# Performance work log

Hardware: AMD Instinct MI355X
Metric: run time of the kernel (lower is better)

Reference implementation:

```python
import jax, jax.numpy as jnp
import numpy as np

N_NODES = 12000
N_EDGES = 384000
F_IN = 128       # num_features
D = 64           # latent_dim (hidden_dim), num_gc_layers = 1
H_DEC = 64       # ceil(F_IN / 2)
BN_EPS = 1e-4


def _gcn_conv(x, W, b, src, dst, n):
    # PyG GCNConv: h = x @ W; add self-loops; sym-normalized scatter-add; + bias
    h = x @ W
    loop = jnp.arange(n)
    s = jnp.concatenate([src, loop])
    d = jnp.concatenate([dst, loop])
    deg = jax.ops.segment_sum(jnp.ones(s.shape[0], dtype=x.dtype), d, num_segments=n)
    dis = jax.lax.rsqrt(deg)  # deg >= 1 thanks to self-loops
    norm = dis[s] * dis[d]    # [E+N]
    out = jax.ops.segment_sum(h[s] * norm[:, None], d, num_segments=n)
    return out + b


def _bn_train(x, gamma, beta):
    # BatchNorm1d, training-mode batch statistics, biased variance, eps=1e-4
    mu = jnp.mean(x, axis=0)
    xc = x - mu
    var = jnp.mean(xc * xc, axis=0)
    return xc * jax.lax.rsqrt(var + BN_EPS) * gamma + beta


def _enc_layer(x, W, b, g, be, src, dst, n):
    # GCNConv -> Sigmoid -> (dropout no-op) -> BatchNorm
    return _bn_train(jax.nn.sigmoid(_gcn_conv(x, W, b, src, dst, n)), g, be)


def setup_inputs() -> dict:
    key = jax.random.key(0)
    ks = jax.random.split(key, 16)
    inp = {
        'x': jax.random.normal(ks[0], (N_NODES, F_IN), dtype=jnp.float32),
        'src': jax.random.randint(ks[1], (N_EDGES,), 0, N_NODES),
        'dst': jax.random.randint(ks[2], (N_EDGES,), 0, N_NODES),
        'batch': jnp.zeros((N_NODES,), dtype=jnp.int32),
        'noise': jax.random.normal(ks[3], (N_NODES, D), dtype=jnp.float32),
        # base_gcn encoder (GCNConv F_IN -> D, BN)
        'W0': jax.random.normal(ks[4], (F_IN, D), dtype=jnp.float32) * 0.08,
        'b0': jnp.zeros((D,), dtype=jnp.float32),
        'g0': jnp.ones((D,), dtype=jnp.float32),
        'be0': jnp.zeros((D,), dtype=jnp.float32),
        # gcn_mean encoder (GCNConv D -> D, BN)
        'Wm': jax.random.normal(ks[5], (D, D), dtype=jnp.float32) * 0.12,
        'bm': jnp.zeros((D,), dtype=jnp.float32),
        'gm': jnp.ones((D,), dtype=jnp.float32),
        'bem': jnp.zeros((D,), dtype=jnp.float32),
        # gcn_logstddev encoder (GCNConv D -> D, BN)
        'Ws': jax.random.normal(ks[6], (D, D), dtype=jnp.float32) * 0.12,
        'bs': jnp.zeros((D,), dtype=jnp.float32),
        'gs': jnp.ones((D,), dtype=jnp.float32),
        'bes': jnp.zeros((D,), dtype=jnp.float32),
        # decoder MLP: Linear(D, H_DEC) -> LeakyReLU -> Linear(H_DEC, F_IN)
        'Dw1': jax.random.normal(ks[7], (D, H_DEC), dtype=jnp.float32) * 0.12,
        'Db1': jnp.zeros((H_DEC,), dtype=jnp.float32),
        'Dw2': jax.random.normal(ks[8], (H_DEC, F_IN), dtype=jnp.float32) * 0.12,
        'Db2': jnp.zeros((F_IN,), dtype=jnp.float32),
    }
    return inp


def reference(x, src, dst, batch, noise,
              W0, b0, g0, be0,
              Wm, bm, gm, bem,
              Ws, bs, gs, bes,
              Dw1, Db1, Dw2, Db2):
    n = x.shape[0]
    hidden = _enc_layer(x, W0, b0, g0, be0, src, dst, n)          # [N, D]
    mean = _enc_layer(hidden, Wm, bm, gm, bem, src, dst, n)       # [N, D]
    logstd = _enc_layer(hidden, Ws, bs, gs, bes, src, dst, n)     # [N, D]
    z = noise * jnp.exp(logstd) + mean                            # reparam trick
    # decoder MLP (LeakyReLU default slope 0.01)
    h = jax.nn.leaky_relu(z @ Dw1 + Db1, negative_slope=0.01)
    reconstructed_x = h @ Dw2 + Db2                               # [N, F_IN]
    A_pred = jax.nn.sigmoid(z @ z.T)                              # [N, N]
    return (reconstructed_x, A_pred)
```

## Files before the change

kernel.cpp:

```cpp
#include <hip/hip_runtime.h>
#include <hip/hip_bf16.h>

#define N_NODES 12000
#define N_EDGES 384000
#define F_INN   128
#define DLAT    64
#define BN_EPS  1e-4f

typedef __attribute__((ext_vector_type(8))) short bf16x8;
typedef __attribute__((ext_vector_type(4))) float f32x4;

__device__ __forceinline__ float sigmoidf(float x) { return 1.0f / (1.0f + __expf(-x)); }

__device__ __forceinline__ unsigned short f2bf_rne(float x) {
    unsigned u = __float_as_uint(x);
    unsigned r = (u + 0x7fffu + ((u >> 16) & 1u)) >> 16;
    return (unsigned short)r;
}
__device__ __forceinline__ float bf2f(unsigned short h) {
    return __uint_as_float((unsigned)h << 16);
}

__global__ void k_init(int* cnt, int* cur, int n) {
    int i = blockIdx.x * blockDim.x + threadIdx.x;
    if (i < n) { cnt[i] = 0; cur[i] = 0; }
}

__global__ void k_count(const int* dst, int* cnt, int e) {
    int i = blockIdx.x * blockDim.x + threadIdx.x;
    if (i < e) atomicAdd(&cnt[dst[i]], 1);
}

__global__ void k_scan(const int* __restrict__ cnt, int* __restrict__ offs,
                       float* __restrict__ dis, int n) {
    __shared__ int wsum[16];
    int tid = threadIdx.x;
    int base = tid * 12;
    int v[12];
    int s = 0;
#pragma unroll
    for (int q = 0; q < 12; q++) {
        int i = base + q;
        v[q] = (i < n) ? cnt[i] : 0;
        s += v[q];
        if (i < n) dis[i] = rsqrtf((float)(v[q] + 1));
    }
    int lane = tid & 63, w = tid >> 6;
    int ps = s;
#pragma unroll
    for (int o = 1; o < 64; o <<= 1) {
        int t2 = __shfl_up(ps, o, 64);
        if (lane >= o) ps += t2;
    }
    if (lane == 63) wsum[w] = ps;
    __syncthreads();
    if (tid == 0) {
        int acc = 0;
        for (int i = 0; i < 16; i++) { int t2 = wsum[i]; wsum[i] = acc; acc += t2; }
    }
    __syncthreads();
    int acc = wsum[w] + ps - s;
#pragma unroll
    for (int q = 0; q < 12; q++) {
        int i = base + q;
        if (i < n) offs[i] = acc;
        acc += v[q];
        if (i == n - 1) offs[n] = acc;
    }
}

__global__ void k_scatter(const int* src, const int* dst, const int* offs, int* cur,
                          int* ssrc, int e) {
    int i = blockIdx.x * blockDim.x + threadIdx.x;
    if (i < e) {
        int d = dst[i];
        int p = atomicAdd(&cur[d], 1);
        ssrc[offs[d] + p] = src[i];
    }
}

__global__ void k_mm(const float* __restrict__ X, int n, int K,
                     const float* __restrict__ Wa, int Ma,
                     const float* __restrict__ Wb, int Mb,
                     float* __restrict__ out) {
    __shared__ float Wl[8192];
    int M = Ma + Mb;
    for (int idx = threadIdx.x; idx < K * M; idx += blockDim.x) {
        int k = idx / M, m = idx % M;
        Wl[idx] = (m < Ma) ? Wa[k * Ma + m] : Wb[k * Mb + (m - Ma)];
    }
    __syncthreads();
    int rpb = blockDim.x / M;
    int r = blockIdx.x * rpb + threadIdx.x / M;
    int m = threadIdx.x % M;
    if (r >= n) return;
    const float* xr = X + (size_t)r * K;
    float acc = 0.f;
    for (int k = 0; k < K; k++) acc += xr[k] * Wl[k * M + m];
    out[(size_t)r * M + m] = acc;
}

__global__ void k_agg(const float* __restrict__ h, const float* __restrict__ dis,
                      const int* __restrict__ offs, const int* __restrict__ ssrc,
                      const float* __restrict__ ba, const float* __restrict__ bb, int Ma,
                      float* __restrict__ out, int dim, int n) {
    int t = blockIdx.x * blockDim.x + threadIdx.x;
    int node = t / dim;
    if (node >= n) return;
    int f = t - node * dim;
    float di = dis[node];
    float acc = h[(size_t)node * dim + f] * di;
    int e0 = offs[node], e1 = offs[node + 1];
    int j = e0;
    for (; j + 3 < e1; j += 4) {
        int s0 = ssrc[j], s1 = ssrc[j + 1], s2 = ssrc[j + 2], s3 = ssrc[j + 3];
        acc += h[(size_t)s0 * dim + f] * dis[s0];
        acc += h[(size_t)s1 * dim + f] * dis[s1];
        acc += h[(size_t)s2 * dim + f] * dis[s2];
        acc += h[(size_t)s3 * dim + f] * dis[s3];
    }
    for (; j < e1; j++) {
        int s = ssrc[j];
        acc += h[(size_t)s * dim + f] * dis[s];
    }
    float bias = (f < Ma) ? ba[f] : bb[f - Ma];
    out[(size_t)node * dim + f] = sigmoidf(acc * di + bias);
}

#define STATS_BLOCKS 64
__global__ void k_stats1(const float* __restrict__ act, int dim, int n,
                         float* __restrict__ part) {
    int rpb = 256 / dim;
    int c = threadIdx.x % dim;
    int rloc = threadIdx.x / dim;
    float s = 0.f, s2 = 0.f;
    for (int r = blockIdx.x * rpb + rloc; r < n; r += STATS_BLOCKS * rpb) {
        float v = act[(size_t)r * dim + c];
        s += v; s2 += v * v;
    }
    __shared__ float sh[512];
    sh[threadIdx.x] = s; sh[256 + threadIdx.x] = s2;
    __syncthreads();
    if (rloc == 0) {
        for (int q = 1; q < rpb; q++) {
            s += sh[q * dim + c];
            s2 += sh[256 + q * dim + c];
        }
        part[(size_t)(blockIdx.x * dim + c) * 2] = s;
        part[(size_t)(blockIdx.x * dim + c) * 2 + 1] = s2;
    }
}

__global__ void k_stats2(const float* __restrict__ part, int dim, int n,
                         float* __restrict__ mu, float* __restrict__ var) {
    int c = threadIdx.x;
    if (c >= dim) return;
    float s = 0.f, s2 = 0.f;
    for (int q = 0; q < STATS_BLOCKS; q++) {
        s += part[(size_t)(q * dim + c) * 2];
        s2 += part[(size_t)(q * dim + c) * 2 + 1];
    }
    float m = s / n;
    mu[c] = m;
    var[c] = s2 / n - m * m;
}

__global__ void k_bnapply(const float* __restrict__ in, float* __restrict__ out,
                          const float* __restrict__ mu, const float* __restrict__ var,
                          const float* __restrict__ g, const float* __restrict__ be,
                          int dim, size_t total) {
    size_t i = (size_t)blockIdx.x * blockDim.x + threadIdx.x;
    if (i >= total) return;
    int f = (int)(i % dim);
    out[i] = (in[i] - mu[f]) * rsqrtf(var[f] + BN_EPS) * g[f] + be[f];
}

__global__ void k_z(const float* __restrict__ act2, const float* __restrict__ noise,
                    const float* __restrict__ mu, const float* __restrict__ var,
                    const float* __restrict__ gm, const float* __restrict__ bem,
                    const float* __restrict__ gs, const float* __restrict__ bes,
                    float* __restrict__ z, unsigned short* __restrict__ zh,
                    unsigned short* __restrict__ zl, int n) {
    int i = blockIdx.x * blockDim.x + threadIdx.x;
    if (i >= 12032 * 64) return;
    int row = i >> 6, j = i & 63;
    if (row >= n) { zh[i] = 0; zl[i] = 0; return; }
    const float* ar = act2 + (size_t)row * 128;
    float m  = (ar[j]      - mu[j])      * rsqrtf(var[j]      + BN_EPS) * gm[j] + bem[j];
    float ls = (ar[j + 64] - mu[j + 64]) * rsqrtf(var[j + 64] + BN_EPS) * gs[j] + bes[j];
    float zv = noise[i] * __expf(ls) + m;
    z[i] = zv;
    unsigned short h = f2bf_rne(zv);
    zh[i] = h;
    zl[i] = f2bf_rne(zv - bf2f(h));
}

__global__ void k_dec(const float* __restrict__ z,
                      const float* __restrict__ W1, const float* __restrict__ B1,
                      const float* __restrict__ W2, const float* __restrict__ B2,
                      float* __restrict__ out, int n) {
    __shared__ float w1[64 * 64];
    __shared__ float w2[64 * 128];
    __shared__ float zl[16 * 64];
    __shared__ float hl[16 * 64];
    int t = threadIdx.x;
    int row0 = blockIdx.x * 16;
    {
        const float4* W14 = (const float4*)W1;
        const float4* W24 = (const float4*)W2;
        for (int i = t; i < 1024; i += 256) ((float4*)w1)[i] = W14[i];
        for (int i = t; i < 2048; i += 256) ((float4*)w2)[i] = W24[i];
        ((float4*)zl)[t] = ((const float4*)(z + (size_t)row0 * 64))[t];
    }
    __syncthreads();
    {
        int hc = t & 63, rg = t >> 6;
        float a0 = B1[hc], a1 = a0, a2 = a0, a3 = a0;
        int rb = rg * 4;
        for (int k = 0; k < 64; k++) {
            float wv = w1[k * 64 + hc];
            a0 += zl[(rb + 0) * 64 + k] * wv;
            a1 += zl[(rb + 1) * 64 + k] * wv;
            a2 += zl[(rb + 2) * 64 + k] * wv;
            a3 += zl[(rb + 3) * 64 + k] * wv;
        }
        hl[(rb + 0) * 64 + hc] = a0 > 0.f ? a0 : 0.01f * a0;
        hl[(rb + 1) * 64 + hc] = a1 > 0.f ? a1 : 0.01f * a1;
        hl[(rb + 2) * 64 + hc] = a2 > 0.f ? a2 : 0.01f * a2;
        hl[(rb + 3) * 64 + hc] = a3 > 0.f ? a3 : 0.01f * a3;
    }
    __syncthreads();
    {
        int oc = t & 127, rg = t >> 7;
        float o[8];
#pragma unroll
        for (int i = 0; i < 8; i++) o[i] = B2[oc];
        int rb = rg * 8;
        for (int k = 0; k < 64; k++) {
            float wv = w2[k * 128 + oc];
#pragma unroll
            for (int i = 0; i < 8; i++) o[i] += hl[(rb + i) * 64 + k] * wv;
        }
#pragma unroll
        for (int i = 0; i < 8; i++)
            out[(size_t)(row0 + rb + i) * 128 + oc] = o[i];
    }
}

#define TN2 94
__global__ __launch_bounds__(256, 2) void k_apred(const unsigned short* __restrict__ zh,
                                                  const unsigned short* __restrict__ zl,
                                                  float* __restrict__ out, int n) {
    __shared__ __align__(16) unsigned short si_h[128 * 64];
    __shared__ __align__(16) unsigned short si_l[128 * 64];
    __shared__ __align__(16) unsigned short sj_h[128 * 64];
    __shared__ __align__(16) unsigned short sj_l[128 * 64];

    int bj = blockIdx.x, bi = blockIdx.y;
    int i0 = bi * 128, j0 = bj * 128;
    int t = threadIdx.x;

    auto stage = [&](const unsigned short* __restrict__ g, unsigned short* s, int row0) {
#pragma unroll
        for (int q = 0; q < 4; q++) {
            int u = q * 256 + t;
            int row = u >> 3, c16 = u & 7;
            int c16s = c16 ^ (row & 7);
            *(float4*)((char*)s + row * 128 + c16s * 16) =
                *(const float4*)(g + (size_t)(row0 + row) * 64 + c16 * 8);
        }
    };
    stage(zh, si_h, i0);
    stage(zl, si_l, i0);
    stage(zh, sj_h, j0);
    stage(zl, sj_l, j0);
    __syncthreads();

    int wave = t >> 6, lane = t & 63;
    int wr = wave >> 1, wc = wave & 1;
    int lrow = lane & 15;
    int kg   = lane >> 4;

    auto frag = [&](const unsigned short* s, int tr, int kc) -> bf16x8 {
        int c16s = (kc * 4 + kg) ^ (tr & 7);
        return *(const bf16x8*)((const char*)s + tr * 128 + c16s * 16);
    };

    f32x4 acc[4][4] = {};

#pragma unroll
    for (int kc = 0; kc < 2; kc++) {
        bf16x8 ah[4], al[4], bh[4], bl[4];
#pragma unroll
        for (int f = 0; f < 4; f++) {
            int tra = wr * 64 + f * 16 + lrow;
            ah[f] = frag(si_h, tra, kc);
            al[f] = frag(si_l, tra, kc);
            int trb = wc * 64 + f * 16 + lrow;
            bh[f] = frag(sj_h, trb, kc);
            bl[f] = frag(sj_l, trb, kc);
        }
#pragma unroll
        for (int fi = 0; fi < 4; fi++)
#pragma unroll
            for (int fj = 0; fj < 4; fj++) {
                acc[fi][fj] = __builtin_amdgcn_mfma_f32_16x16x32_bf16(
                    ah[fi], bh[fj], acc[fi][fj], 0, 0, 0);
                acc[fi][fj] = __builtin_amdgcn_mfma_f32_16x16x32_bf16(
                    ah[fi], bl[fj], acc[fi][fj], 0, 0, 0);
                acc[fi][fj] = __builtin_amdgcn_mfma_f32_16x16x32_bf16(
                    al[fi], bh[fj], acc[fi][fj], 0, 0, 0);
            }
    }

#pragma unroll
    for (int fi = 0; fi < 4; fi++)
#pragma unroll
        for (int fj = 0; fj < 4; fj++)
#pragma unroll
            for (int q = 0; q < 4; q++)
                acc[fi][fj][q] = sigmoidf(acc[fi][fj][q]);

    int colb = j0 + wc * 64;
#pragma unroll
    for (int fi = 0; fi < 4; fi++) {
#pragma unroll
        for (int q = 0; q < 4; q++) {
            int r = i0 + wr * 64 + fi * 16 + kg * 4 + q;
            if (r < n) {
                float* orow = out + (size_t)r * n + colb;
#pragma unroll
                for (int fj = 0; fj < 4; fj++) {
                    int c = fj * 16 + lrow;
                    if (colb + c < n) orow[c] = acc[fi][fj][q];
                }
            }
        }
    }
}

extern "C" void kernel_launch(void* const* d_in, const int* in_sizes, int n_in,
                              void* d_out, int out_size, void* d_ws, size_t ws_size,
                              hipStream_t stream) {
    const float* x     = (const float*)d_in[0];
    const int*   src   = (const int*)d_in[1];
    const int*   dst   = (const int*)d_in[2];
    const float* noise = (const float*)d_in[4];
    const float* W0  = (const float*)d_in[5];
    const float* b0  = (const float*)d_in[6];
    const float* g0  = (const float*)d_in[7];
    const float* be0 = (const float*)d_in[8];
    const float* Wm  = (const float*)d_in[9];
    const float* bm  = (const float*)d_in[10];
    const float* gm  = (const float*)d_in[11];
    const float* bem = (const float*)d_in[12];
    const float* Ws  = (const float*)d_in[13];
    const float* bs  = (const float*)d_in[14];
    const float* gs  = (const float*)d_in[15];
    const float* bes = (const float*)d_in[16];
    const float* Dw1 = (const float*)d_in[17];
    const float* Db1 = (const float*)d_in[18];
    const float* Dw2 = (const float*)d_in[19];
    const float* Db2 = (const float*)d_in[20];
    float* out = (float*)d_out;

    const int n = N_NODES, e = N_EDGES;

    int*   cnt  = (int*)d_ws;
    int*   offs = (int*)d_ws + 12032;
    int*   cur  = (int*)d_ws + 24064;
    int*   ssrc = (int*)d_ws + 36096;
    float* dis  = (float*)d_ws + 420096;
    float* mu   = (float*)d_ws + 432128;
    float* var  = (float*)d_ws + 432384;
    float* part = (float*)d_ws + 432640;
    float* bufA = (float*)d_ws + 449024;
    float* bufB = bufA + (size_t)N_NODES * 128;
    float* zbuf = bufB;
    unsigned short* zhbuf = (unsigned short*)((float*)d_ws + 3521024);
    unsigned short* zlbuf = (unsigned short*)((float*)d_ws + 3906048);

    k_init<<<(n + 255) / 256, 256, 0, stream>>>(cnt, cur, n);
    k_count<<<(e + 255) / 256, 256, 0, stream>>>(dst, cnt, e);
    k_scan<<<1, 1024, 0, stream>>>(cnt, offs, dis, n);
    k_scatter<<<(e + 255) / 256, 256, 0, stream>>>(src, dst, offs, cur, ssrc, e);

    k_mm<<<n / 4, 256, 0, stream>>>(x, n, F_INN, W0, DLAT, nullptr, 0, bufA);
    k_agg<<<(n * DLAT) / 256, 256, 0, stream>>>(bufA, dis, offs, ssrc, b0, nullptr, DLAT,
                                                bufB, DLAT, n);
    k_stats1<<<STATS_BLOCKS, 256, 0, stream>>>(bufB, DLAT, n, part);
    k_stats2<<<1, 64, 0, stream>>>(part, DLAT, n, mu, var);
    k_bnapply<<<(n * DLAT) / 256, 256, 0, stream>>>(bufB, bufA, mu, var, g0, be0, DLAT,
                                                    (size_t)n * DLAT);

    k_mm<<<n / 2, 256, 0, stream>>>(bufA, n, DLAT, Wm, DLAT, Ws, DLAT, bufB);
    k_agg<<<(n * 128) / 256, 256, 0, stream>>>(bufB, dis, offs, ssrc, bm, bs, DLAT,
                                               bufA, 128, n);
    k_stats1<<<STATS_BLOCKS, 256, 0, stream>>>(bufA, 128, n, part);
    k_stats2<<<1, 128, 0, stream>>>(part, 128, n, mu, var);

    k_z<<<(12032 * 64) / 256, 256, 0, stream>>>(bufA, noise, mu, var, gm, bem, gs, bes,
                                                zbuf, zhbuf, zlbuf, n);

    k_dec<<<n / 16, 256, 0, stream>>>(zbuf, Dw1, Db1, Dw2, Db2, out, n);

    {
        dim3 grid(TN2, TN2);
        k_apred<<<grid, 256, 0, stream>>>(zhbuf, zlbuf, out + (size_t)n * F_INN, n);
    }
}
```

Measured before the change: 952.6 us.

## Fuse BatchNorm apply into matmul and z/decoder kernels, use atomic stats

Drops the separate stats-finalize, BN-apply and z kernels. BN statistics are accumulated with atomics into a zeroed buffer, the first BN is folded into the following matmul's input load, and the second BN plus the reparameterization are computed inside the decoder kernel, which also writes the bf16 hi/lo z arrays. The large A_pred output now uses nontemporal stores. This cuts kernel launches and intermediate round trips to memory, but float atomics make the reduction order nondeterministic.

```diff
diff --git a/kernel.cpp b/kernel.cpp
--- a/kernel.cpp
+++ b/kernel.cpp
@@ -21,9 +21,16 @@
     return __uint_as_float((unsigned)h << 16);
 }
 
-__global__ void k_init(int* cnt, int* cur, int n) {
+__global__ void k_init(int* cnt, int* cur, float* sA, float* sB,
+                       unsigned short* zh, unsigned short* zl, int n) {
     int i = blockIdx.x * blockDim.x + threadIdx.x;
     if (i < n) { cnt[i] = 0; cur[i] = 0; }
+    if (i < 128) sA[i] = 0.f;
+    if (i < 256) sB[i] = 0.f;
+    if (i < 2048) {
+        zh[12000 * 64 + i] = 0;
+        zl[12000 * 64 + i] = 0;
+    }
 }
 
 __global__ void k_count(const int* dst, int* cnt, int e) {
@@ -98,6 +105,39 @@
     float acc = 0.f;
     for (int k = 0; k < K; k++) acc += xr[k] * Wl[k * M + m];
     out[(size_t)r * M + m] = acc;
+}
+
+__global__ void k_mm2bn(const float* __restrict__ X,
+                        const float* __restrict__ sums,
+                        const float* __restrict__ g0, const float* __restrict__ be0,
+                        const float* __restrict__ Wa, const float* __restrict__ Wb,
+                        float* __restrict__ out, int n) {
+    __shared__ float Wl[64 * 128];
+    __shared__ float bna[64], bnc[64];
+    __shared__ float xs[2 * 64];
+    int t = threadIdx.x;
+    for (int idx = t; idx < 64 * 128; idx += 256) {
+        int k = idx >> 7, m = idx & 127;
+        Wl[idx] = (m < 64) ? Wa[k * 64 + m] : Wb[k * 64 + (m - 64)];
+    }
+    if (t < 64) {
+        float mu = sums[t] / n;
+        float var = sums[64 + t] / n - mu * mu;
+        float a = rsqrtf(var + BN_EPS) * g0[t];
+        bna[t] = a;
+        bnc[t] = be0[t] - mu * a;
+    }
+    __syncthreads();
+    if (t < 128) {
+        int rr = t >> 6, k = t & 63;
+        xs[rr * 64 + k] = X[(size_t)(blockIdx.x * 2 + rr) * 64 + k] * bna[k] + bnc[k];
+    }
+    __syncthreads();
+    int r_loc = t >> 7, m = t & 127;
+    int r = blockIdx.x * 2 + r_loc;
+    float acc = 0.f;
+    for (int k = 0; k < 64; k++) acc += xs[r_loc * 64 + k] * Wl[k * 128 + m];
+    out[(size_t)r * 128 + m] = acc;
 }
 
 __global__ void k_agg(const float* __restrict__ h, const float* __restrict__ dis,
@@ -129,7 +169,7 @@
 
 #define STATS_BLOCKS 64
 __global__ void k_stats1(const float* __restrict__ act, int dim, int n,
-                         float* __restrict__ part) {
+                         float* __restrict__ sums) {
     int rpb = 256 / dim;
     int c = threadIdx.x % dim;
     int rloc = threadIdx.x / dim;
@@ -146,63 +186,24 @@
             s += sh[q * dim + c];
             s2 += sh[256 + q * dim + c];
         }
-        part[(size_t)(blockIdx.x * dim + c) * 2] = s;
-        part[(size_t)(blockIdx.x * dim + c) * 2 + 1] = s2;
-    }
-}
-
-__global__ void k_stats2(const float* __restrict__ part, int dim, int n,
-                         float* __restrict__ mu, float* __restrict__ var) {
-    int c = threadIdx.x;
-    if (c >= dim) return;
-    float s = 0.f, s2 = 0.f;
-    for (int q = 0; q < STATS_BLOCKS; q++) {
-        s += part[(size_t)(q * dim + c) * 2];
-        s2 += part[(size_t)(q * dim + c) * 2 + 1];
-    }
-    float m = s / n;
-    mu[c] = m;
-    var[c] = s2 / n - m * m;
-}
-
-__global__ void k_bnapply(const float* __restrict__ in, float* __restrict__ out,
-                          const float* __restrict__ mu, const float* __restrict__ var,
-                          const float* __restrict__ g, const float* __restrict__ be,
-                          int dim, size_t total) {
-    size_t i = (size_t)blockIdx.x * blockDim.x + threadIdx.x;
-    if (i >= total) return;
-    int f = (int)(i % dim);
-    out[i] = (in[i] - mu[f]) * rsqrtf(var[f] + BN_EPS) * g[f] + be[f];
-}
-
-__global__ void k_z(const float* __restrict__ act2, const float* __restrict__ noise,
-                    const float* __restrict__ mu, const float* __restrict__ var,
-                    const float* __restrict__ gm, const float* __restrict__ bem,
-                    const float* __restrict__ gs, const float* __restrict__ bes,
-                    float* __restrict__ z, unsigned short* __restrict__ zh,
-                    unsigned short* __restrict__ zl, int n) {
-    int i = blockIdx.x * blockDim.x + threadIdx.x;
-    if (i >= 12032 * 64) return;
-    int row = i >> 6, j = i & 63;
-    if (row >= n) { zh[i] = 0; zl[i] = 0; return; }
-    const float* ar = act2 + (size_t)row * 128;
-    float m  = (ar[j]      - mu[j])      * rsqrtf(var[j]      + BN_EPS) * gm[j] + bem[j];
-    float ls = (ar[j + 64] - mu[j + 64]) * rsqrtf(var[j + 64] + BN_EPS) * gs[j] + bes[j];
-    float zv = noise[i] * __expf(ls) + m;
-    z[i] = zv;
-    unsigned short h = f2bf_rne(zv);
-    zh[i] = h;
-    zl[i] = f2bf_rne(zv - bf2f(h));
-}
-
-__global__ void k_dec(const float* __restrict__ z,
-                      const float* __restrict__ W1, const float* __restrict__ B1,
-                      const float* __restrict__ W2, const float* __restrict__ B2,
-                      float* __restrict__ out, int n) {
+        atomicAdd(&sums[c], s);
+        atomicAdd(&sums[dim + c], s2);
+    }
+}
+
+__global__ void k_zdec(const float* __restrict__ act2, const float* __restrict__ noise,
+                       const float* __restrict__ sums,
+                       const float* __restrict__ gm, const float* __restrict__ bem,
+                       const float* __restrict__ gs, const float* __restrict__ bes,
+                       const float* __restrict__ W1, const float* __restrict__ B1,
+                       const float* __restrict__ W2, const float* __restrict__ B2,
+                       unsigned short* __restrict__ zh, unsigned short* __restrict__ zl,
+                       float* __restrict__ out, int n) {
     __shared__ float w1[64 * 64];
     __shared__ float w2[64 * 128];
-    __shared__ float zl[16 * 64];
+    __shared__ float zs[16 * 64];
     __shared__ float hl[16 * 64];
+    __shared__ float bnS[128], bnC[128];
     int t = threadIdx.x;
     int row0 = blockIdx.x * 16;
     {
@@ -210,7 +211,35 @@
         const float4* W24 = (const float4*)W2;
         for (int i = t; i < 1024; i += 256) ((float4*)w1)[i] = W14[i];
         for (int i = t; i < 2048; i += 256) ((float4*)w2)[i] = W24[i];
-        ((float4*)zl)[t] = ((const float4*)(z + (size_t)row0 * 64))[t];
+    }
+    if (t < 128) {
+        float mu = sums[t] / n;
+        float var = sums[128 + t] / n - mu * mu;
+        float rs = rsqrtf(var + BN_EPS);
+        float g  = (t < 64) ? gm[t] : gs[t - 64];
+        float be = (t < 64) ? bem[t] : bes[t - 64];
+        float a = rs * g;
+        bnS[t] = a;
+        bnC[t] = be - mu * a;
+    }
+    __syncthreads();
+    {
+        int base = t * 4;
+        int row = base >> 6, j0 = base & 63;
+        const float* ar = act2 + (size_t)(row0 + row) * 128;
+        const float* nr = noise + (size_t)(row0 + row) * 64;
+#pragma unroll
+        for (int q = 0; q < 4; q++) {
+            int j = j0 + q;
+            float m  = ar[j]      * bnS[j]      + bnC[j];
+            float ls = ar[64 + j] * bnS[64 + j] + bnC[64 + j];
+            float zv = nr[j] * __expf(ls) + m;
+            zs[row * 64 + j] = zv;
+            unsigned short h = f2bf_rne(zv);
+            size_t gi = (size_t)(row0 + row) * 64 + j;
+            zh[gi] = h;
+            zl[gi] = f2bf_rne(zv - bf2f(h));
+        }
     }
     __syncthreads();
     {
@@ -219,10 +248,10 @@
         int rb = rg * 4;
         for (int k = 0; k < 64; k++) {
             float wv = w1[k * 64 + hc];
-            a0 += zl[(rb + 0) * 64 + k] * wv;
-            a1 += zl[(rb + 1) * 64 + k] * wv;
-            a2 += zl[(rb + 2) * 64 + k] * wv;
-            a3 += zl[(rb + 3) * 64 + k] * wv;
+            a0 += zs[(rb + 0) * 64 + k] * wv;
+            a1 += zs[(rb + 1) * 64 + k] * wv;
+            a2 += zs[(rb + 2) * 64 + k] * wv;
+            a3 += zs[(rb + 3) * 64 + k] * wv;
         }
         hl[(rb + 0) * 64 + hc] = a0 > 0.f ? a0 : 0.01f * a0;
         hl[(rb + 1) * 64 + hc] = a1 > 0.f ? a1 : 0.01f * a1;
@@ -332,7 +361,8 @@
 #pragma unroll
                 for (int fj = 0; fj < 4; fj++) {
                     int c = fj * 16 + lrow;
-                    if (colb + c < n) orow[c] = acc[fi][fj][q];
+                    if (colb + c < n)
+                        __builtin_nontemporal_store(acc[fi][fj][q], &orow[c]);
                 }
             }
         }
@@ -371,16 +401,14 @@
     int*   cur  = (int*)d_ws + 24064;
     int*   ssrc = (int*)d_ws + 36096;
     float* dis  = (float*)d_ws + 420096;
-    float* mu   = (float*)d_ws + 432128;
-    float* var  = (float*)d_ws + 432384;
-    float* part = (float*)d_ws + 432640;
+    float* sA   = (float*)d_ws + 432128;
+    float* sB   = (float*)d_ws + 432384;
     float* bufA = (float*)d_ws + 449024;
     float* bufB = bufA + (size_t)N_NODES * 128;
-    float* zbuf = bufB;
     unsigned short* zhbuf = (unsigned short*)((float*)d_ws + 3521024);
     unsigned short* zlbuf = (unsigned short*)((float*)d_ws + 3906048);
 
-    k_init<<<(n + 255) / 256, 256, 0, stream>>>(cnt, cur, n);
+    k_init<<<(n + 255) / 256, 256, 0, stream>>>(cnt, cur, sA, sB, zhbuf, zlbuf, n);
     k_count<<<(e + 255) / 256, 256, 0, stream>>>(dst, cnt, e);
     k_scan<<<1, 1024, 0, stream>>>(cnt, offs, dis, n);
     k_scatter<<<(e + 255) / 256, 256, 0, stream>>>(src, dst, offs, cur, ssrc, e);
@@ -388,21 +416,15 @@
     k_mm<<<n / 4, 256, 0, stream>>>(x, n, F_INN, W0, DLAT, nullptr, 0, bufA);
     k_agg<<<(n * DLAT) / 256, 256, 0, stream>>>(bufA, dis, offs, ssrc, b0, nullptr, DLAT,
                                                 bufB, DLAT, n);
-    k_stats1<<<STATS_BLOCKS, 256, 0, stream>>>(bufB, DLAT, n, part);
-    k_stats2<<<1, 64, 0, stream>>>(part, DLAT, n, mu, var);
-    k_bnapply<<<(n * DLAT) / 256, 256, 0, stream>>>(bufB, bufA, mu, var, g0, be0, DLAT,
-                                                    (size_t)n * DLAT);
-
-    k_mm<<<n / 2, 256, 0, stream>>>(bufA, n, DLAT, Wm, DLAT, Ws, DLAT, bufB);
-    k_agg<<<(n * 128) / 256, 256, 0, stream>>>(bufB, dis, offs, ssrc, bm, bs, DLAT,
-                                               bufA, 128, n);
-    k_stats1<<<STATS_BLOCKS, 256, 0, stream>>>(bufA, 128, n, part);
-    k_stats2<<<1, 128, 0, stream>>>(part, 128, n, mu, var);
-
-    k_z<<<(12032 * 64) / 256, 256, 0, stream>>>(bufA, noise, mu, var, gm, bem, gs, bes,
-                                                zbuf, zhbuf, zlbuf, n);
-
-    k_dec<<<n / 16, 256, 0, stream>>>(zbuf, Dw1, Db1, Dw2, Db2, out, n);
+    k_stats1<<<STATS_BLOCKS, 256, 0, stream>>>(bufB, DLAT, n, sA);
+
+    k_mm2bn<<<n / 2, 256, 0, stream>>>(bufB, sA, g0, be0, Wm, Ws, bufA, n);
+    k_agg<<<(n * 128) / 256, 256, 0, stream>>>(bufA, dis, offs, ssrc, bm, bs, DLAT,
+                                               bufB, 128, n);
+    k_stats1<<<STATS_BLOCKS, 256, 0, stream>>>(bufB, 128, n, sB);
+
+    k_zdec<<<n / 16, 256, 0, stream>>>(bufB, noise, sB, gm, bem, gs, bes,
+                                       Dw1, Db1, Dw2, Db2, zhbuf, zlbuf, out, n);
 
     {
         dim3 grid(TN2, TN2);
```

Result: faster. 902.2 us (-5.3%).
